# Kernel tuning notes

Measured on AMD Instinct MI355X. Metric: run time of the kernel, lower is better.

## Reference

```python
import jax, jax.numpy as jnp
import numpy as np
import math

# dims matching init_kwargs
B, N, CS, CZ = 1, 512, 384, 128
H, C, PQ, PV = 8, 128, 8, 8
INF, EPS = 1e5, 1e-8

# ---- quaternion / motor helpers (PGA motor encoded as [qw,qx,qy,qz,tx,ty,tz,0]) ----

def quat_conj(q):
    return q * jnp.array([1.0, -1.0, -1.0, -1.0], q.dtype)

def quat_mul(a, b):
    aw, ax, ay, az = jnp.split(a, 4, -1)
    bw, bx, by, bz = jnp.split(b, 4, -1)
    return jnp.concatenate([
        aw*bw - ax*bx - ay*by - az*bz,
        aw*bx + ax*bw + ay*bz - az*by,
        aw*by - ax*bz + ay*bw + az*bx,
        aw*bz + ax*by - ay*bx + az*bw], -1)

def quat_rotate(q, v):
    qv = q[..., 1:]
    uv = jnp.cross(qv, v)
    uuv = jnp.cross(qv, uv)
    return v + 2.0 * (q[..., :1] * uv + uuv)

def point_trafo(p, q, t):
    # p [...,K,3]; rigid transform by frame motor, homogeneous 4-vector out
    pp = quat_rotate(q, p) + t
    return jnp.concatenate([pp, jnp.ones_like(pp[..., :1])], -1)

def mv_transform(mv, q, t):
    # versor sandwich on a 16-dim multivector: three rotatable 3-vector blocks,
    # the point block (7:10, weight at 10) also translates; slots 0 and 10:16 invariant
    s0 = mv[..., 0:1]
    v1 = quat_rotate(q, mv[..., 1:4])
    v2 = quat_rotate(q, mv[..., 4:7])
    w = mv[..., 10:11]
    p = quat_rotate(q, mv[..., 7:10]) + w * t
    return jnp.concatenate([s0, v1, v2, p, mv[..., 10:16]], -1)

def mv_transform_inv(mv, q, t):
    qc = quat_conj(q)
    s0 = mv[..., 0:1]
    v1 = quat_rotate(qc, mv[..., 1:4])
    v2 = quat_rotate(qc, mv[..., 4:7])
    w = mv[..., 10:11]
    p = quat_rotate(qc, mv[..., 7:10] - w * t)
    return jnp.concatenate([s0, v1, v2, p, mv[..., 10:16]], -1)


def _forward(s, g, z, T, mask, W_q, b_q, W_kv, b_kv, W_qp, b_qp, W_kp, b_kp,
             W_vg, b_vg, W_mg, W_b, b_b, W_dz, b_dz, head_weights,
             softmax_weights, W_out, b_out, W_geo):
    T8 = T[..., :8]                                      # extract_motor
    qn = T8[..., :4]
    qn = qn / jnp.sqrt(jnp.sum(qn**2, -1, keepdims=True) + EPS)
    tr = T8[..., 4:7]

    q = (s @ W_q + b_q).reshape(B, N, H, C)
    kv = (s @ W_kv + b_kv).reshape(B, N, H, 2 * C)
    k, v = kv[..., :C], kv[..., C:]

    def make_pts(W, bb):
        # split into 3 chunks + stack(dim=-1) == reshape(...,3,HP).swapaxes
        p = (s @ W + bb).reshape(B, N, 3, H * PQ).swapaxes(-1, -2)  # [B,N,HP,3]
        p4 = point_trafo(p, qn[:, :, None, :], tr[:, :, None, :])
        return p4.reshape(B, N, H, PQ, 4)

    q_pts = make_pts(W_qp, b_qp)
    k_pts = make_pts(W_kp, b_kp)

    v_g = (s @ W_vg + b_vg).reshape(B, N, PV, 16)
    v_g = jnp.einsum('oi,bnic->bnoc', W_mg,
                     jnp.concatenate([v_g, g], -2)).reshape(B, N, H, PV, 16)

    bias = jnp.einsum('bijz,zh->bhij', z, W_b) + b_b[None, :, None, None]
    a = jnp.einsum('bihc,bjhc->bhij', q, k) * math.sqrt(1.0 / (3 * C))
    a = a + math.sqrt(1.0 / 3.0) * bias

    disp = q_pts[:, :, None, :, :, :3] - k_pts[:, None, :, :, :, :3]  # [B,N,N,H,P,3]
    pt = jnp.sum(disp**2, -1)                                         # [B,N,N,H,P]
    hw = jax.nn.softplus(head_weights) * math.sqrt(1.0 / (3 * (PQ * 9.0 / 2)))
    pt = -0.5 * jnp.sum(pt * hw[None, None, None, :, None], -1)       # [B,N,N,H]

    sq_mask = INF * (mask[:, :, None] * mask[:, None, :] - 1.0)
    a = a + pt.transpose(0, 3, 1, 2) + sq_mask[:, None]
    a = jax.nn.softmax(softmax_weights[None, :, None, None] * a, axis=-1)

    o = jnp.einsum('bhij,bjhc->bihc', a, v)                           # [B,N,H,C]

    qb, tb = qn[:, :, None, None, :], tr[:, :, None, None, :]
    vg_glob = mv_transform(v_g, qb, tb)
    o_g = jnp.einsum('bhij,bjhpc->bihpc', a, vg_glob)
    o_g = mv_transform_inv(o_g, qb, tb)                               # [B,N,H,PV,16]
    n1 = jnp.sqrt(jnp.sum(o_g[..., :10]**2, -1) + EPS)
    n2 = jnp.sqrt(jnp.sum(o_g[..., 10:]**2, -1) + EPS)
    o_g_norm = jnp.stack([n1, n2], -1)                                # [B,N,H,PV,2]

    # local relative frame features (8 per head)
    q_rel = quat_mul(quat_conj(qn)[:, :, None, :], qn[:, None, :, :])
    t_rel = quat_rotate(quat_conj(qn)[:, :, None, :], tr[:, None, :, :] - tr[:, :, None, :])
    rel = jnp.concatenate([q_rel, t_rel, jnp.zeros_like(t_rel[..., :1])], -1)  # [B,N,N,8]
    o_rel = jnp.einsum('bhij,bijc->bihc', a, rel)

    o_pair = jnp.einsum('bhij,bijc->bihc', a, z @ W_dz + b_dz)        # [B,N,H,CZ//4]

    feats = jnp.concatenate([o_pair, o, o_rel,
                             o_g.reshape(B, N, H, PV * 16),
                             o_g_norm.reshape(B, N, H, PV * 2)], -1).reshape(B, N, -1)
    s_out = feats @ W_out + b_out                                     # [B,N,CS]
    g_out = jnp.einsum('oi,bnic->bnoc', W_geo, o_g.reshape(B, N, H * PV, 16))
    return s_out, g_out


def setup_inputs() -> dict:
    key = jax.random.key(0)
    ks = jax.random.split(key, 32)
    def rn(i, shape, sc=1.0):
        return sc * jax.random.normal(ks[i], shape, jnp.float32)
    s = rn(0, (B, N, CS))
    g = rn(1, (B, N, PV, 16))
    z = rn(2, (B, N, N, CZ))
    Traw = rn(3, (B, N, 16))
    qn = Traw[..., :4]
    qn = qn / jnp.sqrt(jnp.sum(qn**2, -1, keepdims=True) + 1e-8)
    T = Traw.at[..., :4].set(qn).at[..., 4:7].multiply(3.0).at[..., 7:].set(0.0)
    mask = jnp.ones((B, N), jnp.float32)
    w = 0.02
    CAT = H * (CZ // 4 + C + 8 + PV * 18)   # 2496
    return dict(
        s=s, g=g, z=z, T=T, mask=mask,
        W_q=rn(4, (CS, H * C), w), b_q=jnp.zeros((H * C,), jnp.float32),
        W_kv=rn(5, (CS, 2 * H * C), w), b_kv=jnp.zeros((2 * H * C,), jnp.float32),
        W_qp=rn(6, (CS, H * PQ * 3), w), b_qp=jnp.zeros((H * PQ * 3,), jnp.float32),
        W_kp=rn(7, (CS, H * PQ * 3), w), b_kp=jnp.zeros((H * PQ * 3,), jnp.float32),
        W_vg=rn(8, (CS, PV * 16), w), b_vg=jnp.zeros((PV * 16,), jnp.float32),
        W_mg=rn(9, (H * PV, 2 * PV), 0.1),
        W_b=rn(10, (CZ, H), w), b_b=jnp.zeros((H,), jnp.float32),
        W_dz=rn(11, (CZ, CZ // 4), w), b_dz=jnp.zeros((CZ // 4,), jnp.float32),
        head_weights=-2.0 + 0.3 * rn(12, (H,)),
        softmax_weights=jnp.ones((H,), jnp.float32) + 0.1 * rn(13, (H,)),
        W_out=rn(14, (CAT, CS), w), b_out=jnp.zeros((CS,), jnp.float32),
        W_geo=rn(15, (PV, H * PV), 0.1))


def reference(s, g, z, T, mask, W_q, b_q, W_kv, b_kv, W_qp, b_qp, W_kp, b_kp,
              W_vg, b_vg, W_mg, W_b, b_b, W_dz, b_dz, head_weights,
              softmax_weights, W_out, b_out, W_geo):
    return _forward(s, g, z, T, mask, W_q, b_q, W_kv, b_kv, W_qp, b_qp, W_kp,
                    b_kp, W_vg, b_vg, W_mg, W_b, b_b, W_dz, b_dz, head_weights,
                    softmax_weights, W_out, b_out, W_geo)
```

## Files before the change

### kernel.cpp

```cpp
#include <hip/hip_runtime.h>
#include <math.h>

#define NN 512
#define CSD 384
#define CZD 128
#define HD 8
#define CD 128
#define EPSV 1e-8f
#define INFV 100000.0f

#define OFF_QN    ((size_t)0)
#define OFF_TR    ((size_t)2048)
#define OFF_ROWT  ((size_t)4096)
#define OFF_COLT  ((size_t)8192)
#define OFF_SB    ((size_t)12288)
#define OFF_QBUF  ((size_t)45056)
#define OFF_KV    ((size_t)569344)
#define OFF_QPR   ((size_t)1617920)
#define OFF_KPR   ((size_t)1716224)
#define OFF_VGR   ((size_t)1814528)
#define OFF_ZB    ((size_t)1880064)
#define OFF_A     ((size_t)3977216)
#define OFF_AMH   ((size_t)6074368)
#define OFF_AML   ((size_t)7122944)
#define OFF_UH    ((size_t)8171520)
#define OFF_UL    ((size_t)8499200)
#define OFF_VH    ((size_t)8826880)
#define OFF_VL    ((size_t)9154560)
#define OFF_VPH   ((size_t)9482240)
#define OFF_VPL   ((size_t)10006528)
#define OFF_OB0   ((size_t)10530816)
#define OFF_OB1   ((size_t)11055104)
#define OFF_OG0   ((size_t)11579392)
#define OFF_OG1   ((size_t)12103680)
#define OFF_FH    ((size_t)12627968)
#define OFF_FL    ((size_t)13266944)
#define OFF_PS    ((size_t)13905920)
#define OFF_SH    ((size_t)15085568)
#define OFF_SL    ((size_t)15183872)
#define OFF_WTH   ((size_t)15282176)
#define OFF_WTL   ((size_t)15970304)
#define OFF_WOH   ((size_t)16658432)
#define OFF_WOL   ((size_t)17137664)

typedef __attribute__((ext_vector_type(4))) float f32x4;
typedef __attribute__((ext_vector_type(8))) short bf16x8;
typedef __attribute__((ext_vector_type(4))) short s16x4;
typedef unsigned short u16;

__device__ __forceinline__ void qrot(const float q[4], const float* v, float* out) {
    float qw = q[0], qx = q[1], qy = q[2], qz = q[3];
    float ux = qy*v[2] - qz*v[1];
    float uy = qz*v[0] - qx*v[2];
    float uz = qx*v[1] - qy*v[0];
    float uux = qy*uz - qz*uy;
    float uuy = qz*ux - qx*uz;
    float uuz = qx*uy - qy*ux;
    out[0] = v[0] + 2.0f*(qw*ux + uux);
    out[1] = v[1] + 2.0f*(qw*uy + uuy);
    out[2] = v[2] + 2.0f*(qw*uz + uuz);
}

__device__ __forceinline__ void cvt2(float x, u16& h, u16& lo) {
    unsigned u = __float_as_uint(x);
    unsigned r = (u + 0x7FFFu + ((u >> 16) & 1u)) >> 16;
    h = (u16)r;
    float hf = __uint_as_float(r << 16);
    float lf = x - hf;
    unsigned u2 = __float_as_uint(lf);
    unsigned r2 = (u2 + 0x7FFFu + ((u2 >> 16) & 1u)) >> 16;
    lo = (u16)r2;
}
__device__ __forceinline__ float bf2f(u16 h) { return __uint_as_float((unsigned)h << 16); }

#define MFMA3(acc, avh, avl, bvh, bvl) \
    acc = __builtin_amdgcn_mfma_f32_16x16x32_bf16(avh, bvh, acc, 0, 0, 0); \
    acc = __builtin_amdgcn_mfma_f32_16x16x32_bf16(avh, bvl, acc, 0, 0, 0); \
    acc = __builtin_amdgcn_mfma_f32_16x16x32_bf16(avl, bvh, acc, 0, 0, 0);


__global__ __launch_bounds__(256) void k_split(
    const float* __restrict__ s, const float* __restrict__ W_q, const float* __restrict__ W_kv,
    const float* __restrict__ W_qp, const float* __restrict__ W_kp, const float* __restrict__ W_vg,
    const float* __restrict__ W_out,
    u16* __restrict__ sh_, u16* __restrict__ sl_,
    u16* __restrict__ WTh, u16* __restrict__ WTl,
    u16* __restrict__ WOh, u16* __restrict__ WOl)
{
    __shared__ float tile[64*68];
    int task = blockIdx.z, bx = blockIdx.x, by = blockIdx.y, t = threadIdx.x;
    if (task == 0) {
        if (by >= 6) return;
        const float* W; int ldn, sn0;
        if (bx < 16)      { W = W_q;  ldn = 1024; sn0 = bx*64; }
        else if (bx < 48) { W = W_kv; ldn = 2048; sn0 = (bx-16)*64; }
        else if (bx < 51) { W = W_qp; ldn = 192;  sn0 = (bx-48)*64; }
        else if (bx < 54) { W = W_kp; ldn = 192;  sn0 = (bx-51)*64; }
        else              { W = W_vg; ldn = 128;  sn0 = (bx-54)*64; }
        int k0 = by*64;
        #pragma unroll
        for (int lp = 0; lp < 4; lp++) {
            int kk = (t>>4) + lp*16, nn = (t&15)*4;
            float4 v = *(const float4*)(W + (size_t)(k0+kk)*ldn + sn0 + nn);
            tile[kk*68+nn]=v.x; tile[kk*68+nn+1]=v.y; tile[kk*68+nn+2]=v.z; tile[kk*68+nn+3]=v.w;
        }
        __syncthreads();
        #pragma unroll
        for (int lp = 0; lp < 4; lp++) {
            int nn = (t>>4) + lp*16, kk4 = (t&15)*4;
            s16x4 vh, vl;
            #pragma unroll
            for (int e = 0; e < 4; e++) {
                u16 h, lo; cvt2(tile[(kk4+e)*68 + nn], h, lo);
                vh[e] = (short)h; vl[e] = (short)lo;
            }
            size_t o = (size_t)(bx*64 + nn)*384 + k0 + kk4;
            *(s16x4*)(WTh + o) = vh;
            *(s16x4*)(WTl + o) = vl;
        }
    } else if (task == 1) {
        if (bx >= 6 || by >= 39) return;
        int n0 = bx*64, k0 = by*64;
        #pragma unroll
        for (int lp = 0; lp < 4; lp++) {
            int kk = (t>>4) + lp*16, nn = (t&15)*4;
            float4 v = *(const float4*)(W_out + (size_t)(k0+kk)*384 + n0 + nn);
            tile[kk*68+nn]=v.x; tile[kk*68+nn+1]=v.y; tile[kk*68+nn+2]=v.z; tile[kk*68+nn+3]=v.w;
        }
        __syncthreads();
        #pragma unroll
        for (int lp = 0; lp < 4; lp++) {
            int nn = (t>>4) + lp*16, kk4 = (t&15)*4;
            s16x4 vh, vl;
            #pragma unroll
            for (int e = 0; e < 4; e++) {
                u16 h, lo; cvt2(tile[(kk4+e)*68 + nn], h, lo);
                vh[e] = (short)h; vl[e] = (short)lo;
            }
            size_t o = (size_t)(n0 + nn)*2496 + k0 + kk4;
            *(s16x4*)(WOh + o) = vh;
            *(s16x4*)(WOl + o) = vl;
        }
    } else {
        if (bx >= 8 || by >= 6) return;
        int m0 = bx*64, k0 = by*64;
        #pragma unroll
        for (int lp = 0; lp < 4; lp++) {
            int row = (t>>4) + lp*16, c4 = (t&15)*4;
            float4 v = *(const float4*)(s + (size_t)(m0+row)*384 + k0 + c4);
            s16x4 vh, vl;
            u16 h, lo;
            cvt2(v.x,h,lo); vh[0]=(short)h; vl[0]=(short)lo;
            cvt2(v.y,h,lo); vh[1]=(short)h; vl[1]=(short)lo;
            cvt2(v.z,h,lo); vh[2]=(short)h; vl[2]=(short)lo;
            cvt2(v.w,h,lo); vh[3]=(short)h; vl[3]=(short)lo;
            size_t o = (size_t)(m0+row)*384 + k0 + c4;
            *(s16x4*)(sh_ + o) = vh;
            *(s16x4*)(sl_ + o) = vl;
        }
    }
}

__global__ __launch_bounds__(256) void k_proj_all(
    const u16* __restrict__ sh_, const u16* __restrict__ sl_,
    const u16* __restrict__ WTh, const u16* __restrict__ WTl,
    const float* __restrict__ b_q,  float* __restrict__ qbuf,
    const float* __restrict__ b_kv, float* __restrict__ kvb,
    const float* __restrict__ b_qp, float* __restrict__ qpr,
    const float* __restrict__ b_kp, float* __restrict__ kpr,
    const float* __restrict__ b_vg, float* __restrict__ vgr)
{
    int ny = blockIdx.y;
    const float* bias; float* C; int N, n0, base;
    if (ny < 16)      { bias=b_q;  C=qbuf; N=1024; n0=ny*64;      base=0; }
    else if (ny < 48) { bias=b_kv; C=kvb;  N=2048; n0=(ny-16)*64; base=1024; }
    else if (ny < 51) { bias=b_qp; C=qpr;  N=192;  n0=(ny-48)*64; base=3072; }
    else if (ny < 54) { bias=b_kp; C=kpr;  N=192;  n0=(ny-51)*64; base=3264; }
    else              { bias=b_vg; C=vgr;  N=128;  n0=(ny-54)*64; base=3456; }
    int m0 = blockIdx.x*64;
    int t = threadIdx.x, w = t>>6, l = t&63, g = l>>4, li = l&15;
    const u16* Ah = sh_ + (size_t)(m0 + w*16 + li)*384 + g*8;
    const u16* Al = sl_ + (size_t)(m0 + w*16 + li)*384 + g*8;
    const u16* Bh0 = WTh + (size_t)(base + n0 + li)*384 + g*8;
    const u16* Bl0 = WTl + (size_t)(base + n0 + li)*384 + g*8;
    f32x4 acc[4] = {};
    for (int ks = 0; ks < 12; ks++) {
        bf16x8 avh = *(const bf16x8*)(Ah + ks*32);
        bf16x8 avl = *(const bf16x8*)(Al + ks*32);
        #pragma unroll
        for (int c = 0; c < 4; c++) {
            bf16x8 bvh = *(const bf16x8*)(Bh0 + (size_t)c*16*384 + ks*32);
            bf16x8 bvl = *(const bf16x8*)(Bl0 + (size_t)c*16*384 + ks*32);
            MFMA3(acc[c], avh, avl, bvh, bvl);
        }
    }
    #pragma unroll
    for (int c = 0; c < 4; c++) {
        int col = n0 + c*16 + li;
        float bb = bias[col];
        #pragma unroll
        for (int r = 0; r < 4; r++) {
            int row = m0 + w*16 + g*4 + r;
            C[(size_t)row*N + col] = acc[c][r] + bb;
        }
    }
}

__global__ __launch_bounds__(256) void k_geo(
    const float* __restrict__ T,
    const float* __restrict__ qpr, const float* __restrict__ kpr,
    const float* __restrict__ vgr, const float* __restrict__ g,
    const float* __restrict__ W_mg,
    const float* __restrict__ qbuf, const float* __restrict__ kvb,
    const float* __restrict__ hwraw, const float* __restrict__ b_b,
    float* __restrict__ qn, float* __restrict__ tr,
    u16* __restrict__ Uh, u16* __restrict__ Ul,
    u16* __restrict__ Vh, u16* __restrict__ Vl,
    float* __restrict__ rowt, float* __restrict__ colt,
    u16* __restrict__ Vph, u16* __restrict__ Vpl)
{
    __shared__ float s_q[4];
    __shared__ float s_t[3];
    __shared__ float s_qpts[192], s_kpts[192];
    __shared__ float s_Qsq[8], s_Ksq[8];
    int n = blockIdx.x, t = threadIdx.x;
    if (t == 0) {
        float q0=T[n*16+0], q1=T[n*16+1], q2=T[n*16+2], q3=T[n*16+3];
        float inv = 1.0f/sqrtf(q0*q0+q1*q1+q2*q2+q3*q3 + EPSV);
        float a0=q0*inv, a1=q1*inv, a2=q2*inv, a3=q3*inv;
        s_q[0]=a0; s_q[1]=a1; s_q[2]=a2; s_q[3]=a3;
        float u0=T[n*16+4], u1=T[n*16+5], u2=T[n*16+6];
        s_t[0]=u0; s_t[1]=u1; s_t[2]=u2;
        qn[n*4+0]=a0; qn[n*4+1]=a1; qn[n*4+2]=a2; qn[n*4+3]=a3;
        tr[n*3+0]=u0; tr[n*3+1]=u1; tr[n*3+2]=u2;
    }
    __syncthreads();
    float q[4]={s_q[0],s_q[1],s_q[2],s_q[3]};
    float t0=s_t[0], t1=s_t[1], t2=s_t[2];
    if (t < 128) {
        int m = t & 63;
        const float* raw = (t < 64) ? qpr : kpr;
        float p[3] = {raw[n*192 + m], raw[n*192 + 64 + m], raw[n*192 + 128 + m]};
        float r[3]; qrot(q,p,r);
        r[0]+=t0; r[1]+=t1; r[2]+=t2;
        float* dp = (t<64) ? s_qpts : s_kpts;
        dp[m*3+0]=r[0]; dp[m*3+1]=r[1]; dp[m*3+2]=r[2];
        float ss = r[0]*r[0]+r[1]*r[1]+r[2]*r[2];
        ss += __shfl_down(ss,4,8);
        ss += __shfl_down(ss,2,8);
        ss += __shfl_down(ss,1,8);
        if ((m&7)==0) ((t<64)?s_Qsq:s_Ksq)[m>>3] = ss;
    } else if (t < 192) {
        int o = t - 128;
        float in[16];
        #pragma unroll
        for (int c=0;c<16;c++){
            float acc=0.0f;
            #pragma unroll
            for (int i=0;i<8;i++)  acc += W_mg[o*16+i]*vgr[n*128+i*16+c];
            #pragma unroll
            for (int i=8;i<16;i++) acc += W_mg[o*16+i]*g[n*128+(i-8)*16+c];
            in[c]=acc;
        }
        float out[16];
        out[0]=in[0];
        qrot(q,in+1,out+1);
        qrot(q,in+4,out+4);
        float w=in[10];
        qrot(q,in+7,out+7);
        out[7]+=w*t0; out[8]+=w*t1; out[9]+=w*t2;
        #pragma unroll
        for (int c=10;c<16;c++) out[c]=in[c];
        int h=o>>3, pp=o&7;
        size_t vb = ((size_t)(h*512+n))*256 + 128 + pp*16;
        #pragma unroll
        for (int c=0;c<16;c++) {
            u16 hh, ll; cvt2(out[c], hh, ll);
            Vph[vb+c]=hh; Vpl[vb+c]=ll;
        }
    }
    #pragma unroll
    for (int l=0;l<4;l++){
        int f = t + l*256; int h = f>>7, c = f&127;
        u16 hh, ll; cvt2(kvb[(size_t)n*2048 + h*256 + 128 + c], hh, ll);
        Vph[((size_t)(h*512+n))*256 + c] = hh;
        Vpl[((size_t)(h*512+n))*256 + c] = ll;
    }
    __syncthreads();
    #pragma unroll
    for (int h = 0; h < 8; h++) {
        float hwv = log1pf(expf(hwraw[h])) * 0.09622504486493763f;
        if (t < 160) {
            float u, v;
            if (t < 128) {
                u = 0.05103103630798287f * qbuf[(size_t)n*1024 + h*128 + t];
                v = kvb[(size_t)n*2048 + h*256 + t];
            } else if (t < 152) {
                int d = t - 128;
                u = hwv * s_qpts[h*24 + d];
                v = s_kpts[h*24 + d];
            } else { u = 0.0f; v = 0.0f; }
            size_t o = ((size_t)h*512 + n)*160 + t;
            u16 hh, ll;
            cvt2(u, hh, ll); Uh[o]=hh; Ul[o]=ll;
            cvt2(v, hh, ll); Vh[o]=hh; Vl[o]=ll;
        }
        if (t == 160) rowt[h*512+n] = -0.5f*hwv*s_Qsq[h] + 0.5773502691896258f*b_b[h] - INFV;
        if (t == 161) colt[h*512+n] = -0.5f*hwv*s_Ksq[h];
    }
}

__global__ __launch_bounds__(128) void k_zb(const float* __restrict__ z,
        const float* __restrict__ W_b, float* __restrict__ zb) {
    __shared__ float zt[64*132];
    __shared__ float part[8*64];
    int i = blockIdx.x, j0 = blockIdx.y*64;
    int t = threadIdx.x;
    #pragma unroll
    for (int l = 0; l < 16; l++) {
        int f = t + l*128;
        int row = f >> 5, c4 = (f & 31) << 2;
        float4 v = *(const float4*)(z + ((size_t)(i*NN) + j0 + row)*CZD + c4);
        *(float4*)(zt + row*132 + c4) = v;
    }
    __syncthreads();
    int w = t >> 6, j = t & 63;
    int cbase = w*64;
    float acc[8] = {};
    #pragma unroll
    for (int c16 = 0; c16 < 16; c16++) {
        float4 v = *(const float4*)(zt + j*132 + cbase + c16*4);
        int c = cbase + c16*4;
        #pragma unroll
        for (int h = 0; h < 8; h++)
            acc[h] += v.x*W_b[(c+0)*8+h] + v.y*W_b[(c+1)*8+h]
                    + v.z*W_b[(c+2)*8+h] + v.w*W_b[(c+3)*8+h];
    }
    if (w == 1) {
        #pragma unroll
        for (int h = 0; h < 8; h++) part[h*64 + j] = acc[h];
    }
    __syncthreads();
    if (w == 0) {
        #pragma unroll
        for (int h = 0; h < 8; h++)
            zb[((size_t)h*512 + i)*512 + j0 + j] = acc[h] + part[h*64 + j];
    }
}

__global__ __launch_bounds__(256) void k_scorefill(
        const u16* __restrict__ Uh, const u16* __restrict__ Ul,
        const u16* __restrict__ Vh, const u16* __restrict__ Vl,
        const float* __restrict__ rowt, const float* __restrict__ colt,
        const float* __restrict__ zb, const float* __restrict__ mask,
        const float* __restrict__ sw, float* __restrict__ Am) {
    int h = blockIdx.z;
    int m0 = blockIdx.x*64, n0 = blockIdx.y*64;
    int t = threadIdx.x, w = t>>6, l = t&63, g = l>>4, li = l&15;
    const u16* Ah = Uh + ((size_t)h*512 + m0 + w*16 + li)*160 + g*8;
    const u16* Al = Ul + ((size_t)h*512 + m0 + w*16 + li)*160 + g*8;
    const u16* Bh0 = Vh + ((size_t)h*512 + n0 + li)*160 + g*8;
    const u16* Bl0 = Vl + ((size_t)h*512 + n0 + li)*160 + g*8;
    f32x4 acc[4] = {};
    #pragma unroll
    for (int ks = 0; ks < 5; ks++) {
        bf16x8 avh = *(const bf16x8*)(Ah + ks*32);
        bf16x8 avl = *(const bf16x8*)(Al + ks*32);
        #pragma unroll
        for (int c = 0; c < 4; c++) {
            bf16x8 bvh = *(const bf16x8*)(Bh0 + (size_t)c*16*160 + ks*32);
            bf16x8 bvl = *(const bf16x8*)(Bl0 + (size_t)c*16*160 + ks*32);
            MFMA3(acc[c], avh, avl, bvh, bvl);
        }
    }
    float swh = sw[h];
    #pragma unroll
    for (int c = 0; c < 4; c++) {
        int j = n0 + c*16 + li;
        float ct = colt[h*512 + j];
        float mj = mask[j];
        #pragma unroll
        for (int r = 0; r < 4; r++) {
            int i = m0 + w*16 + g*4 + r;
            float rt = rowt[h*512 + i];
            float mi = mask[i]*INFV;
            float zv = zb[((size_t)h*512 + i)*512 + j];
            Am[((size_t)h*512 + i)*512 + j] =
                (acc[c][r] + rt + ct + 0.5773502691896258f*zv + mi*mj)*swh;
        }
    }
}

__global__ __launch_bounds__(256) void k_softmax(const float* __restrict__ Am,
        u16* __restrict__ Amh, u16* __restrict__ Aml,
        const float* __restrict__ qn, const float* __restrict__ tr, float* __restrict__ S) {
    __shared__ float red[8];
    __shared__ float sred[4][8];
    int row = blockIdx.x;
    const float* p = Am + (size_t)row*512;
    int t = threadIdx.x;
    float x0 = p[t], x1 = p[t+256];
    float m = fmaxf(x0, x1);
    #pragma unroll
    for (int o = 32; o > 0; o >>= 1) m = fmaxf(m, __shfl_xor(m, o));
    int wv = t >> 6, ln = t & 63;
    if (ln == 0) red[wv] = m;
    __syncthreads();
    m = fmaxf(fmaxf(red[0], red[1]), fmaxf(red[2], red[3]));
    float e0 = expf(x0 - m), e1 = expf(x1 - m);
    float sm = e0 + e1;
    #pragma unroll
    for (int o = 32; o > 0; o >>= 1) sm += __shfl_xor(sm, o);
    __syncthreads();
    if (ln == 0) red[4 + wv] = sm;
    __syncthreads();
    float inv = 1.0f / (red[4]+red[5]+red[6]+red[7]);
    float a0 = e0*inv, a1 = e1*inv;
    u16 hh, ll;
    cvt2(a0, hh, ll); Amh[(size_t)row*512 + t] = hh;     Aml[(size_t)row*512 + t] = ll;
    cvt2(a1, hh, ll); Amh[(size_t)row*512 + t+256] = hh; Aml[(size_t)row*512 + t+256] = ll;
    float4 q0 = *(const float4*)(qn + t*4);
    float4 q1 = *(const float4*)(qn + (t+256)*4);
    float acc[8];
    acc[0] = a0*q0.x + a1*q1.x;
    acc[1] = a0*q0.y + a1*q1.y;
    acc[2] = a0*q0.z + a1*q1.z;
    acc[3] = a0*q0.w + a1*q1.w;
    acc[4] = a0*tr[t*3+0] + a1*tr[(t+256)*3+0];
    acc[5] = a0*tr[t*3+1] + a1*tr[(t+256)*3+1];
    acc[6] = a0*tr[t*3+2] + a1*tr[(t+256)*3+2];
    acc[7] = a0 + a1;
    #pragma unroll
    for (int c = 0; c < 8; c++) {
        #pragma unroll
        for (int o = 32; o > 0; o >>= 1) acc[c] += __shfl_xor(acc[c], o);
    }
    if (ln == 0) {
        #pragma unroll
        for (int c = 0; c < 8; c++) sred[wv][c] = acc[c];
    }
    __syncthreads();
    if (t < 8) {
        int h = row >> 9, i = row & 511;
        S[i*64 + h*8 + t] = sred[0][t]+sred[1][t]+sred[2][t]+sred[3][t];
    }
}

__global__ __launch_bounds__(256) void k_apply(
        const u16* __restrict__ Amh, const u16* __restrict__ Aml,
        const u16* __restrict__ Vph, const u16* __restrict__ Vpl,
        float* __restrict__ ob0, float* __restrict__ ob1,
        float* __restrict__ og0, float* __restrict__ og1) {
    __shared__ u16 sBh[2][64*48];
    __shared__ u16 sBl[2][64*48];
    int m0 = blockIdx.x*64;
    int n0 = blockIdx.y*64;
    int h = blockIdx.z & 7, js = blockIdx.z >> 3;
    int t = threadIdx.x, w = t>>6, l = t&63, g = l>>4, li = l&15;
    int jl = t>>3, c8 = (t&7)*8;
    int jsw = jl ^ (((c8>>3)&3)<<3);
    const u16* Ah = Amh + ((size_t)h*512 + m0 + w*16 + li)*512 + js*256 + g*8;
    const u16* Al = Aml + ((size_t)h*512 + m0 + w*16 + li)*512 + js*256 + g*8;
    f32x4 acc[4] = {};
    {
        const u16* srcH = Vph + ((size_t)h*512 + js*256 + jl)*256 + n0 + c8;
        const u16* srcL = Vpl + ((size_t)h*512 + js*256 + jl)*256 + n0 + c8;
        bf16x8 vh = *(const bf16x8*)srcH;
        bf16x8 vl = *(const bf16x8*)srcL;
        #pragma unroll
        for (int e = 0; e < 8; e++) {
            sBh[0][(c8+e)*48 + jsw] = (u16)vh[e];
            sBl[0][(c8+e)*48 + jsw] = (u16)vl[e];
        }
    }
    __syncthreads();
    for (int kc = 0; kc < 8; kc++) {
        int cur = kc & 1;
        if (kc + 1 < 8) {
            int koff = js*256 + (kc+1)*32;
            const u16* srcH = Vph + ((size_t)h*512 + koff + jl)*256 + n0 + c8;
            const u16* srcL = Vpl + ((size_t)h*512 + koff + jl)*256 + n0 + c8;
            bf16x8 vh = *(const bf16x8*)srcH;
            bf16x8 vl = *(const bf16x8*)srcL;
            #pragma unroll
            for (int e = 0; e < 8; e++) {
                sBh[cur^1][(c8+e)*48 + jsw] = (u16)vh[e];
                sBl[cur^1][(c8+e)*48 + jsw] = (u16)vl[e];
            }
        }
        bf16x8 avh = *(const bf16x8*)(Ah + kc*32);
        bf16x8 avl = *(const bf16x8*)(Al + kc*32);
        #pragma unroll
        for (int c = 0; c < 4; c++) {
            int col = c*16 + li;
            int gp = g ^ ((col>>3)&3);
            bf16x8 bvh = *(const bf16x8*)(&sBh[cur][col*48 + gp*8]);
            bf16x8 bvl = *(const bf16x8*)(&sBl[cur][col*48 + gp*8]);
            MFMA3(acc[c], avh, avl, bvh, bvl);
        }
        __syncthreads();
    }
    float* obuf = js ? ob1 : ob0;
    float* og   = js ? og1 : og0;
    #pragma unroll
    for (int c = 0; c < 4; c++) {
        int col = n0 + c*16 + li;
        float* base = (col < 128) ? (obuf + h*128 + col) : (og + h*128 + col - 128);
        #pragma unroll
        for (int r = 0; r < 4; r++) {
            int i = m0 + w*16 + g*4 + r;
            base[(size_t)i*1024] = acc[c][r];
        }
    }
}

__global__ __launch_bounds__(256) void k_azfin(
    const u16* __restrict__ Amh, const u16* __restrict__ Aml, const float* __restrict__ z,
    const float* __restrict__ ob0, const float* __restrict__ ob1,
    const float* __restrict__ og0, const float* __restrict__ og1,
    const float* __restrict__ W_dz, const float* __restrict__ b_dz,
    const float* __restrict__ S, const float* __restrict__ qn, const float* __restrict__ tr,
    const float* __restrict__ W_geo,
    u16* __restrict__ fh, u16* __restrict__ fl, float* __restrict__ outg)
{
    __shared__ float aT[512*8];
    __shared__ float part[3*1024];
    __shared__ float s_az[1024];
    __shared__ float s_og[1024];
    int i = blockIdx.x, t = threadIdx.x;
    #pragma unroll
    for (int l = 0; l < 16; l++) {
        int f = t + l*256;
        int h = f >> 9, j = f & 511;
        size_t idx = ((size_t)h*512 + i)*512 + j;
        aT[j*8 + h] = bf2f(Amh[idx]) + bf2f(Aml[idx]);
    }
    __syncthreads();
    int c2 = t & 63, quarter = t >> 6;
    int jb = quarter*128;
    float acc[8][2] = {};
    for (int j = jb; j < jb+128; j++) {
        float2 zv = *(const float2*)(z + ((size_t)(i*NN) + j)*CZD + c2*2);
        float4 a0 = *(const float4*)(aT + j*8);
        float4 a1 = *(const float4*)(aT + j*8 + 4);
        acc[0][0] += a0.x*zv.x; acc[0][1] += a0.x*zv.y;
        acc[1][0] += a0.y*zv.x; acc[1][1] += a0.y*zv.y;
        acc[2][0] += a0.z*zv.x; acc[2][1] += a0.z*zv.y;
        acc[3][0] += a0.w*zv.x; acc[3][1] += a0.w*zv.y;
        acc[4][0] += a1.x*zv.x; acc[4][1] += a1.x*zv.y;
        acc[5][0] += a1.y*zv.x; acc[5][1] += a1.y*zv.y;
        acc[6][0] += a1.z*zv.x; acc[6][1] += a1.z*zv.y;
        acc[7][0] += a1.w*zv.x; acc[7][1] += a1.w*zv.y;
    }
    if (quarter > 0) {
        #pragma unroll
        for (int h = 0; h < 8; h++) {
            part[(quarter-1)*1024 + h*128 + c2*2 + 0] = acc[h][0];
            part[(quarter-1)*1024 + h*128 + c2*2 + 1] = acc[h][1];
        }
    }
    __syncthreads();
    if (quarter == 0) {
        #pragma unroll
        for (int h = 0; h < 8; h++) {
            #pragma unroll
            for (int d = 0; d < 2; d++) {
                s_az[h*128 + c2*2 + d] = acc[h][d] + part[h*128 + c2*2 + d]
                          + part[1024 + h*128 + c2*2 + d] + part[2048 + h*128 + c2*2 + d];
            }
        }
    }
    __syncthreads();
    size_t fb = (size_t)i*2496;
    u16 hh, ll;
    #pragma unroll
    for (int l = 0; l < 4; l++) {
        int ff = t + l*256; int h = ff>>7, c = ff&127;
        float v = ob0[(size_t)i*1024 + h*128 + c] + ob1[(size_t)i*1024 + h*128 + c];
        cvt2(v, hh, ll); fh[fb + h*312 + 32 + c] = hh; fl[fb + h*312 + 32 + c] = ll;
    }
    {
        int h = t >> 5, cdz = t & 31;
        float a2 = b_dz[cdz];
        #pragma unroll 4
        for (int zc = 0; zc < 128; zc++) a2 += s_az[h*128 + zc]*W_dz[zc*32 + cdz];
        cvt2(a2, hh, ll); fh[fb + h*312 + cdz] = hh; fl[fb + h*312 + cdz] = ll;
    }
    float qc0=qn[i*4], qc1=-qn[i*4+1], qc2=-qn[i*4+2], qc3=-qn[i*4+3];
    float t0=tr[i*3], t1=tr[i*3+1], t2=tr[i*3+2];
    if (t < 64) {
        int h = t >> 3, p = t & 7;
        const float* a0 = og0 + (size_t)i*1024 + h*128 + p*16;
        const float* a1 = og1 + (size_t)i*1024 + h*128 + p*16;
        float in[16];
        #pragma unroll
        for (int c=0;c<16;c++) in[c]=a0[c]+a1[c];
        float qc[4]={qc0,qc1,qc2,qc3};
        float out[16];
        out[0]=in[0];
        qrot(qc,in+1,out+1);
        qrot(qc,in+4,out+4);
        float w=in[10];
        float tmp[3]={in[7]-w*t0, in[8]-w*t1, in[9]-w*t2};
        qrot(qc,tmp,out+7);
        #pragma unroll
        for (int c2x=10;c2x<16;c2x++) out[c2x]=in[c2x];
        float n1=EPSV, n2=EPSV;
        #pragma unroll
        for (int c2x=0;c2x<10;c2x++) n1 += out[c2x]*out[c2x];
        #pragma unroll
        for (int c2x=10;c2x<16;c2x++) n2 += out[c2x]*out[c2x];
        n1=sqrtf(n1); n2=sqrtf(n2);
        #pragma unroll
        for (int c2x=0;c2x<16;c2x++){
            cvt2(out[c2x], hh, ll);
            fh[fb + h*312+168+p*16+c2x] = hh; fl[fb + h*312+168+p*16+c2x] = ll;
            s_og[t*16+c2x]=out[c2x];
        }
// ... 40 lines not shown
    const u16* Al = fl + (size_t)(m0 + w*16 + li)*2496 + kz*416 + g*8;
    const u16* Bh0 = WOh + (size_t)(n0 + li)*2496 + kz*416 + g*8;
    const u16* Bl0 = WOl + (size_t)(n0 + li)*2496 + kz*416 + g*8;
    f32x4 acc[4] = {};
    for (int ks = 0; ks < 13; ks++) {
        bf16x8 avh = *(const bf16x8*)(Ah + ks*32);
        bf16x8 avl = *(const bf16x8*)(Al + ks*32);
        #pragma unroll
        for (int c = 0; c < 4; c++) {
            bf16x8 bvh = *(const bf16x8*)(Bh0 + (size_t)c*16*2496 + ks*32);
            bf16x8 bvl = *(const bf16x8*)(Bl0 + (size_t)c*16*2496 + ks*32);
            MFMA3(acc[c], avh, avl, bvh, bvl);
        }
    }
    float* slab = Ps + (size_t)kz*512*384;
    #pragma unroll
    for (int c = 0; c < 4; c++) {
        int col = n0 + c*16 + li;
        #pragma unroll
        for (int r = 0; r < 4; r++) {
            int row = m0 + w*16 + g*4 + r;
            slab[(size_t)row*CSD + col] = acc[c][r];
        }
    }
}

__global__ __launch_bounds__(256) void k_sout_red(const float* __restrict__ Ps,
        const float* __restrict__ b_out, float* __restrict__ out) {
    int idx = (blockIdx.x*256 + threadIdx.x)*4;
    float4 s = *(const float4*)(b_out + (idx % 384));
    #pragma unroll
    for (int kz = 0; kz < 6; kz++) {
        float4 p = *(const float4*)(Ps + (size_t)kz*196608 + idx);
        s.x += p.x; s.y += p.y; s.z += p.z; s.w += p.w;
    }
    *(float4*)(out + idx) = s;
}


extern "C" void kernel_launch(void* const* d_in, const int* in_sizes, int n_in,
                              void* d_out, int out_size, void* d_ws, size_t ws_size,
                              hipStream_t stream) {
    const float* s     = (const float*)d_in[0];
    const float* g     = (const float*)d_in[1];
    const float* z     = (const float*)d_in[2];
    const float* T     = (const float*)d_in[3];
    const float* mask  = (const float*)d_in[4];
    const float* W_q   = (const float*)d_in[5];
    const float* b_q   = (const float*)d_in[6];
    const float* W_kv  = (const float*)d_in[7];
    const float* b_kv  = (const float*)d_in[8];
    const float* W_qp  = (const float*)d_in[9];
    const float* b_qp  = (const float*)d_in[10];
    const float* W_kp  = (const float*)d_in[11];
    const float* b_kp  = (const float*)d_in[12];
    const float* W_vg  = (const float*)d_in[13];
    const float* b_vg  = (const float*)d_in[14];
    const float* W_mg  = (const float*)d_in[15];
    const float* W_b   = (const float*)d_in[16];
    const float* b_b   = (const float*)d_in[17];
    const float* W_dz  = (const float*)d_in[18];
    const float* b_dz  = (const float*)d_in[19];
    const float* hw    = (const float*)d_in[20];
    const float* sw    = (const float*)d_in[21];
    const float* W_out = (const float*)d_in[22];
    const float* b_out = (const float*)d_in[23];
    const float* W_geo = (const float*)d_in[24];

    float* ws   = (float*)d_ws;
    float* out  = (float*)d_out;

    float* qn   = ws + OFF_QN;
    float* tr   = ws + OFF_TR;
    float* rowt = ws + OFF_ROWT;
    float* colt = ws + OFF_COLT;
    float* Sbuf = ws + OFF_SB;
    float* qbuf = ws + OFF_QBUF;
    float* kvb  = ws + OFF_KV;
    float* qpr  = ws + OFF_QPR;
    float* kpr  = ws + OFF_KPR;
    float* vgr  = ws + OFF_VGR;
    float* zb   = ws + OFF_ZB;
    float* Am   = ws + OFF_A;
    u16* Amh    = (u16*)(ws + OFF_AMH);
    u16* Aml    = (u16*)(ws + OFF_AML);
    u16* Uh     = (u16*)(ws + OFF_UH);
    u16* Ul     = (u16*)(ws + OFF_UL);
    u16* Vh     = (u16*)(ws + OFF_VH);
    u16* Vl     = (u16*)(ws + OFF_VL);
    u16* Vph    = (u16*)(ws + OFF_VPH);
    u16* Vpl    = (u16*)(ws + OFF_VPL);
    float* ob0  = ws + OFF_OB0;
    float* ob1  = ws + OFF_OB1;
    float* og0  = ws + OFF_OG0;
    float* og1  = ws + OFF_OG1;
    u16* fh     = (u16*)(ws + OFF_FH);
    u16* fl     = (u16*)(ws + OFF_FL);
    float* Ps   = ws + OFF_PS;
    u16* sh_    = (u16*)(ws + OFF_SH);
    u16* sl_    = (u16*)(ws + OFF_SL);
    u16* WTh    = (u16*)(ws + OFF_WTH);
    u16* WTl    = (u16*)(ws + OFF_WTL);
    u16* WOh    = (u16*)(ws + OFF_WOH);
    u16* WOl    = (u16*)(ws + OFF_WOL);

    k_split<<<dim3(56,39,3),256,0,stream>>>(s,W_q,W_kv,W_qp,W_kp,W_vg,W_out,
                                            sh_,sl_,WTh,WTl,WOh,WOl);
    k_proj_all<<<dim3(8,56),256,0,stream>>>(sh_,sl_,WTh,WTl,
                                            b_q,qbuf, b_kv,kvb, b_qp,qpr, b_kp,kpr, b_vg,vgr);
    k_geo<<<NN,256,0,stream>>>(T,qpr,kpr,vgr,g,W_mg,qbuf,kvb,hw,b_b,
                               qn,tr,Uh,Ul,Vh,Vl,rowt,colt,Vph,Vpl);
    k_zb<<<dim3(NN,8),128,0,stream>>>(z,W_b,zb);
    k_scorefill<<<dim3(8,8,8),256,0,stream>>>(Uh,Ul,Vh,Vl,rowt,colt,zb,mask,sw,Am);
    k_softmax<<<4096,256,0,stream>>>(Am,Amh,Aml,qn,tr,Sbuf);
    k_apply<<<dim3(8,4,16),256,0,stream>>>(Amh,Aml,Vph,Vpl,ob0,ob1,og0,og1);
    k_azfin<<<NN,256,0,stream>>>(Amh,Aml,z,ob0,ob1,og0,og1,W_dz,b_dz,Sbuf,qn,tr,W_geo,
                                 fh,fl, out + (size_t)NN*CSD);
    k_sout<<<dim3(8,6,6),256,0,stream>>>(fh,fl,WOh,WOl,Ps);
    k_sout_red<<<192,256,0,stream>>>(Ps,b_out,out);
}
```

Measured before the change: 409.6 us.

## Keep attention intermediates in fp32 and split to bf16 hi/lo inside MFMA tiles

Stops writing pre-split bf16 hi/lo copies of U, V, Vp and the attention matrix to global memory. The score and apply kernels now share a templated tile routine that loads fp32 tiles, splits them into hi/lo in LDS and runs three-pass bf16 MFMA with register prefetch. Softmax writes probabilities back in place, which removes the separate hi/lo arrays. k_zb is rewritten to hold W_b in registers and reduce with shuffles. The change trades global traffic for extra conversion work and LDS staging in the GEMM kernels, with the conversion now repeated for every tile that reads the same data.

```diff
diff --git a/kernel.cpp b/kernel.cpp
--- a/kernel.cpp
+++ b/kernel.cpp
@@ -21,27 +21,22 @@
 #define OFF_VGR   ((size_t)1814528)
 #define OFF_ZB    ((size_t)1880064)
 #define OFF_A     ((size_t)3977216)
-#define OFF_AMH   ((size_t)6074368)
-#define OFF_AML   ((size_t)7122944)
-#define OFF_UH    ((size_t)8171520)
-#define OFF_UL    ((size_t)8499200)
-#define OFF_VH    ((size_t)8826880)
-#define OFF_VL    ((size_t)9154560)
-#define OFF_VPH   ((size_t)9482240)
-#define OFF_VPL   ((size_t)10006528)
-#define OFF_OB0   ((size_t)10530816)
-#define OFF_OB1   ((size_t)11055104)
-#define OFF_OG0   ((size_t)11579392)
-#define OFF_OG1   ((size_t)12103680)
-#define OFF_FH    ((size_t)12627968)
-#define OFF_FL    ((size_t)13266944)
-#define OFF_PS    ((size_t)13905920)
-#define OFF_SH    ((size_t)15085568)
-#define OFF_SL    ((size_t)15183872)
-#define OFF_WTH   ((size_t)15282176)
-#define OFF_WTL   ((size_t)15970304)
-#define OFF_WOH   ((size_t)16658432)
-#define OFF_WOL   ((size_t)17137664)
+#define OFF_U     ((size_t)6074368)
+#define OFF_V     ((size_t)6729728)
+#define OFF_VP    ((size_t)7385088)
+#define OFF_OB0   ((size_t)8433664)
+#define OFF_OB1   ((size_t)8957952)
+#define OFF_OG0   ((size_t)9482240)
+#define OFF_OG1   ((size_t)10006528)
+#define OFF_PS    ((size_t)10530816)
+#define OFF_SH    ((size_t)11710464)
+#define OFF_SL    ((size_t)11808768)
+#define OFF_WTH   ((size_t)11907072)
+#define OFF_WTL   ((size_t)12595200)
+#define OFF_WOH   ((size_t)13283328)
+#define OFF_WOL   ((size_t)13762560)
+#define OFF_FH    ((size_t)14241792)
+#define OFF_FL    ((size_t)14880768)
 
 typedef __attribute__((ext_vector_type(4))) float f32x4;
 typedef __attribute__((ext_vector_type(8))) short bf16x8;
@@ -71,12 +66,79 @@
     unsigned r2 = (u2 + 0x7FFFu + ((u2 >> 16) & 1u)) >> 16;
     lo = (u16)r2;
 }
-__device__ __forceinline__ float bf2f(u16 h) { return __uint_as_float((unsigned)h << 16); }
 
 #define MFMA3(acc, avh, avl, bvh, bvl) \
     acc = __builtin_amdgcn_mfma_f32_16x16x32_bf16(avh, bvh, acc, 0, 0, 0); \
     acc = __builtin_amdgcn_mfma_f32_16x16x32_bf16(avh, bvl, acc, 0, 0, 0); \
     acc = __builtin_amdgcn_mfma_f32_16x16x32_bf16(avl, bvh, acc, 0, 0, 0);
+
+__device__ __forceinline__ void stA(short* H, short* L, int row, int k4, float4 v) {
+    u16 h0,l0,h1,l1,h2,l2,h3,l3;
+    cvt2(v.x,h0,l0); cvt2(v.y,h1,l1); cvt2(v.z,h2,l2); cvt2(v.w,h3,l3);
+    s16x4 vh = {(short)h0,(short)h1,(short)h2,(short)h3};
+    s16x4 vl = {(short)l0,(short)l1,(short)l2,(short)l3};
+    *(s16x4*)(H + row*40 + k4) = vh;
+    *(s16x4*)(L + row*40 + k4) = vl;
+}
+__device__ __forceinline__ void stBT(short* H, short* L, int k, int n4, float4 v) {
+    u16 h, lo;
+    cvt2(v.x,h,lo); H[(n4+0)*40+k]=(short)h; L[(n4+0)*40+k]=(short)lo;
+    cvt2(v.y,h,lo); H[(n4+1)*40+k]=(short)h; L[(n4+1)*40+k]=(short)lo;
+    cvt2(v.z,h,lo); H[(n4+2)*40+k]=(short)h; L[(n4+2)*40+k]=(short)lo;
+    cvt2(v.w,h,lo); H[(n4+3)*40+k]=(short)h; L[(n4+3)*40+k]=(short)lo;
+}
+
+template<int BT>
+__device__ __forceinline__ void mfma_tiles(const float* __restrict__ A, int lda,
+                                           const float* __restrict__ B, int ldb,
+                                           int m0, int n0, int k0, int nk,
+                                           f32x4* acc,
+                                           short* Ah, short* Al, short* Bh, short* Bl) {
+    int t = threadIdx.x;
+    int w = t >> 6, l = t & 63, g = l >> 4, li = l & 15;
+    int ar = t >> 3, ak = (t & 7) << 2;
+    const float* Ap0 = A + (size_t)(m0 + ar)*lda + ak;
+    const float* Ap1 = A + (size_t)(m0 + ar + 32)*lda + ak;
+    const float* Bp0; const float* Bp1;
+    int bk = t >> 4, bn = (t & 15) << 2;
+    if (BT) {
+        Bp0 = B + (size_t)(n0 + ar)*ldb + ak;
+        Bp1 = B + (size_t)(n0 + ar + 32)*ldb + ak;
+    } else {
+        Bp0 = B + (size_t)bk*ldb + n0 + bn;
+        Bp1 = B + (size_t)(bk + 16)*ldb + n0 + bn;
+    }
+    float4 a0 = *(const float4*)(Ap0 + k0);
+    float4 a1 = *(const float4*)(Ap1 + k0);
+    float4 b0, b1;
+    if (BT) { b0 = *(const float4*)(Bp0 + k0); b1 = *(const float4*)(Bp1 + k0); }
+    else    { b0 = *(const float4*)(Bp0 + (size_t)k0*ldb); b1 = *(const float4*)(Bp1 + (size_t)k0*ldb); }
+    for (int kc = 0; kc < nk; kc++) {
+        stA(Ah, Al, ar, ak, a0);
+        stA(Ah, Al, ar+32, ak, a1);
+        if (BT) { stA(Bh, Bl, ar, ak, b0); stA(Bh, Bl, ar+32, ak, b1); }
+        else    { stBT(Bh, Bl, bk, bn, b0); stBT(Bh, Bl, bk+16, bn, b1); }
+        __syncthreads();
+        if (kc + 1 < nk) {
+            int kb = k0 + (kc+1)*32;
+            a0 = *(const float4*)(Ap0 + kb);
+            a1 = *(const float4*)(Ap1 + kb);
+            if (BT) { b0 = *(const float4*)(Bp0 + kb); b1 = *(const float4*)(Bp1 + kb); }
+            else { b0 = *(const float4*)(Bp0 + (size_t)kb*ldb); b1 = *(const float4*)(Bp1 + (size_t)kb*ldb); }
+        }
+        int arow = (w*16 + li)*40 + g*8;
+        bf16x8 avh = *(bf16x8*)(Ah + arow);
+        bf16x8 avl = *(bf16x8*)(Al + arow);
+        #pragma unroll
+        for (int c = 0; c < 4; c++) {
+            int brow = (c*16 + li)*40 + g*8;
+            bf16x8 bvh = *(bf16x8*)(Bh + brow);
+            bf16x8 bvl = *(bf16x8*)(Bl + brow);
+            MFMA3(acc[c], avh, avl, bvh, bvl);
+        }
+        __syncthreads();
+    }
+}
 
 
 __global__ __launch_bounds__(256) void k_split(
@@ -214,10 +276,9 @@
     const float* __restrict__ qbuf, const float* __restrict__ kvb,
     const float* __restrict__ hwraw, const float* __restrict__ b_b,
     float* __restrict__ qn, float* __restrict__ tr,
-    u16* __restrict__ Uh, u16* __restrict__ Ul,
-    u16* __restrict__ Vh, u16* __restrict__ Vl,
+    float* __restrict__ U, float* __restrict__ V,
     float* __restrict__ rowt, float* __restrict__ colt,
-    u16* __restrict__ Vph, u16* __restrict__ Vpl)
+    float* __restrict__ Vp)
 {
     __shared__ float s_q[4];
     __shared__ float s_t[3];
@@ -272,19 +333,14 @@
         #pragma unroll
         for (int c=10;c<16;c++) out[c]=in[c];
         int h=o>>3, pp=o&7;
-        size_t vb = ((size_t)(h*512+n))*256 + 128 + pp*16;
-        #pragma unroll
-        for (int c=0;c<16;c++) {
-            u16 hh, ll; cvt2(out[c], hh, ll);
-            Vph[vb+c]=hh; Vpl[vb+c]=ll;
-        }
+        float* vp = Vp + ((size_t)(h*512+n))*256 + 128 + pp*16;
+        #pragma unroll
+        for (int c=0;c<16;c++) vp[c]=out[c];
     }
     #pragma unroll
     for (int l=0;l<4;l++){
         int f = t + l*256; int h = f>>7, c = f&127;
-        u16 hh, ll; cvt2(kvb[(size_t)n*2048 + h*256 + 128 + c], hh, ll);
-        Vph[((size_t)(h*512+n))*256 + c] = hh;
-        Vpl[((size_t)(h*512+n))*256 + c] = ll;
+        Vp[((size_t)(h*512+n))*256 + c] = kvb[(size_t)n*2048 + h*256 + 128 + c];
     }
     __syncthreads();
     #pragma unroll
@@ -300,79 +356,65 @@
                 u = hwv * s_qpts[h*24 + d];
                 v = s_kpts[h*24 + d];
             } else { u = 0.0f; v = 0.0f; }
-            size_t o = ((size_t)h*512 + n)*160 + t;
-            u16 hh, ll;
-            cvt2(u, hh, ll); Uh[o]=hh; Ul[o]=ll;
-            cvt2(v, hh, ll); Vh[o]=hh; Vl[o]=ll;
+            U[((size_t)h*512 + n)*160 + t] = u;
+            V[((size_t)h*512 + n)*160 + t] = v;
         }
         if (t == 160) rowt[h*512+n] = -0.5f*hwv*s_Qsq[h] + 0.5773502691896258f*b_b[h] - INFV;
         if (t == 161) colt[h*512+n] = -0.5f*hwv*s_Ksq[h];
     }
 }
 
-__global__ __launch_bounds__(128) void k_zb(const float* __restrict__ z,
+__global__ __launch_bounds__(256) void k_zb(const float* __restrict__ z,
         const float* __restrict__ W_b, float* __restrict__ zb) {
-    __shared__ float zt[64*132];
-    __shared__ float part[8*64];
-    int i = blockIdx.x, j0 = blockIdx.y*64;
-    int t = threadIdx.x;
-    #pragma unroll
-    for (int l = 0; l < 16; l++) {
-        int f = t + l*128;
-        int row = f >> 5, c4 = (f & 31) << 2;
-        float4 v = *(const float4*)(z + ((size_t)(i*NN) + j0 + row)*CZD + c4);
-        *(float4*)(zt + row*132 + c4) = v;
-    }
-    __syncthreads();
-    int w = t >> 6, j = t & 63;
-    int cbase = w*64;
-    float acc[8] = {};
-    #pragma unroll
-    for (int c16 = 0; c16 < 16; c16++) {
-        float4 v = *(const float4*)(zt + j*132 + cbase + c16*4);
-        int c = cbase + c16*4;
-        #pragma unroll
-        for (int h = 0; h < 8; h++)
-            acc[h] += v.x*W_b[(c+0)*8+h] + v.y*W_b[(c+1)*8+h]
-                    + v.z*W_b[(c+2)*8+h] + v.w*W_b[(c+3)*8+h];
-    }
-    if (w == 1) {
-        #pragma unroll
-        for (int h = 0; h < 8; h++) part[h*64 + j] = acc[h];
-    }
-    __syncthreads();
-    if (w == 0) {
-        #pragma unroll
-        for (int h = 0; h < 8; h++)
-            zb[((size_t)h*512 + i)*512 + j0 + j] = acc[h] + part[h*64 + j];
-    }
-}
-
-__global__ __launch_bounds__(256) void k_scorefill(
-        const u16* __restrict__ Uh, const u16* __restrict__ Ul,
-        const u16* __restrict__ Vh, const u16* __restrict__ Vl,
+    int i = blockIdx.x, j0 = blockIdx.y*128;
+    int t = threadIdx.x, w = t>>6, l = t&63;
+    int gp = l>>4, k = l&15;
+    float wb[8][8];
+    #pragma unroll
+    for (int cc=0;cc<8;cc++){
+        float4 w0 = *(const float4*)(W_b + (k*8+cc)*8);
+        float4 w1 = *(const float4*)(W_b + (k*8+cc)*8 + 4);
+        wb[cc][0]=w0.x; wb[cc][1]=w0.y; wb[cc][2]=w0.z; wb[cc][3]=w0.w;
+        wb[cc][4]=w1.x; wb[cc][5]=w1.y; wb[cc][6]=w1.z; wb[cc][7]=w1.w;
+    }
+    for (int it = 0; it < 8; it++) {
+        int j = j0 + it*16 + w*4 + gp;
+        const float* zp = z + ((size_t)i*512 + j)*128 + k*8;
+        float4 za = *(const float4*)(zp);
+        float4 zb4 = *(const float4*)(zp + 4);
+        float zz[8] = {za.x,za.y,za.z,za.w,zb4.x,zb4.y,zb4.z,zb4.w};
+        float acc[8];
+        #pragma unroll
+        for (int h=0;h<8;h++) acc[h] = zz[0]*wb[0][h];
+        #pragma unroll
+        for (int cc=1;cc<8;cc++)
+            #pragma unroll
+            for (int h=0;h<8;h++) acc[h] += zz[cc]*wb[cc][h];
+        #pragma unroll
+        for (int h=0;h<8;h++) {
+            acc[h] += __shfl_xor(acc[h], 1);
+            acc[h] += __shfl_xor(acc[h], 2);
+            acc[h] += __shfl_xor(acc[h], 4);
+            acc[h] += __shfl_xor(acc[h], 8);
+        }
+        float outv = acc[0];
+        #pragma unroll
+        for (int h=1;h<8;h++) if (k == h) outv = acc[h];
+        if (k < 8) zb[((size_t)k*512 + i)*512 + j] = outv;
+    }
+}
+
+__global__ __launch_bounds__(256) void k_scorefill(const float* __restrict__ U, const float* __restrict__ V,
         const float* __restrict__ rowt, const float* __restrict__ colt,
         const float* __restrict__ zb, const float* __restrict__ mask,
         const float* __restrict__ sw, float* __restrict__ Am) {
+    __shared__ short Ah[64*40], Al[64*40], Bh[64*40], Bl[64*40];
     int h = blockIdx.z;
     int m0 = blockIdx.x*64, n0 = blockIdx.y*64;
-    int t = threadIdx.x, w = t>>6, l = t&63, g = l>>4, li = l&15;
-    const u16* Ah = Uh + ((size_t)h*512 + m0 + w*16 + li)*160 + g*8;
-    const u16* Al = Ul + ((size_t)h*512 + m0 + w*16 + li)*160 + g*8;
-    const u16* Bh0 = Vh + ((size_t)h*512 + n0 + li)*160 + g*8;
-    const u16* Bl0 = Vl + ((size_t)h*512 + n0 + li)*160 + g*8;
     f32x4 acc[4] = {};
-    #pragma unroll
-    for (int ks = 0; ks < 5; ks++) {
-        bf16x8 avh = *(const bf16x8*)(Ah + ks*32);
-        bf16x8 avl = *(const bf16x8*)(Al + ks*32);
-        #pragma unroll
-        for (int c = 0; c < 4; c++) {
-            bf16x8 bvh = *(const bf16x8*)(Bh0 + (size_t)c*16*160 + ks*32);
-            bf16x8 bvl = *(const bf16x8*)(Bl0 + (size_t)c*16*160 + ks*32);
-            MFMA3(acc[c], avh, avl, bvh, bvl);
-        }
-    }
+    mfma_tiles<1>(U + (size_t)h*512*160, 160, V + (size_t)h*512*160, 160,
+                  m0, n0, 0, 5, acc, Ah, Al, Bh, Bl);
+    int t = threadIdx.x, w = t >> 6, l = t & 63, g = l >> 4, li = l & 15;
     float swh = sw[h];
     #pragma unroll
     for (int c = 0; c < 4; c++) {
@@ -391,13 +433,12 @@
     }
 }
 
-__global__ __launch_bounds__(256) void k_softmax(const float* __restrict__ Am,
-        u16* __restrict__ Amh, u16* __restrict__ Aml,
+__global__ __launch_bounds__(256) void k_softmax(float* __restrict__ Am,
         const float* __restrict__ qn, const float* __restrict__ tr, float* __restrict__ S) {
     __shared__ float red[8];
     __shared__ float sred[4][8];
     int row = blockIdx.x;
-    const float* p = Am + (size_t)row*512;
+    float* p = Am + (size_t)row*512;
     int t = threadIdx.x;
     float x0 = p[t], x1 = p[t+256];
     float m = fmaxf(x0, x1);
@@ -416,9 +457,8 @@
     __syncthreads();
     float inv = 1.0f / (red[4]+red[5]+red[6]+red[7]);
     float a0 = e0*inv, a1 = e1*inv;
-    u16 hh, ll;
-    cvt2(a0, hh, ll); Amh[(size_t)row*512 + t] = hh;     Aml[(size_t)row*512 + t] = ll;
-    cvt2(a1, hh, ll); Amh[(size_t)row*512 + t+256] = hh; Aml[(size_t)row*512 + t+256] = ll;
+    p[t] = a0;
+    p[t+256] = a1;
     float4 q0 = *(const float4*)(qn + t*4);
     float4 q1 = *(const float4*)(qn + (t+256)*4);
     float acc[8];
@@ -446,60 +486,17 @@
     }
 }
 
-__global__ __launch_bounds__(256) void k_apply(
-        const u16* __restrict__ Amh, const u16* __restrict__ Aml,
-        const u16* __restrict__ Vph, const u16* __restrict__ Vpl,
-        float* __restrict__ ob0, float* __restrict__ ob1,
+__global__ __launch_bounds__(256) void k_apply(const float* __restrict__ Am,
+        const float* __restrict__ Vp, float* __restrict__ ob0, float* __restrict__ ob1,
         float* __restrict__ og0, float* __restrict__ og1) {
-    __shared__ u16 sBh[2][64*48];
-    __shared__ u16 sBl[2][64*48];
+    __shared__ short Ah[64*40], Al[64*40], Bh[64*40], Bl[64*40];
     int m0 = blockIdx.x*64;
     int n0 = blockIdx.y*64;
     int h = blockIdx.z & 7, js = blockIdx.z >> 3;
-    int t = threadIdx.x, w = t>>6, l = t&63, g = l>>4, li = l&15;
-    int jl = t>>3, c8 = (t&7)*8;
-    int jsw = jl ^ (((c8>>3)&3)<<3);
-    const u16* Ah = Amh + ((size_t)h*512 + m0 + w*16 + li)*512 + js*256 + g*8;
-    const u16* Al = Aml + ((size_t)h*512 + m0 + w*16 + li)*512 + js*256 + g*8;
     f32x4 acc[4] = {};
-    {
-        const u16* srcH = Vph + ((size_t)h*512 + js*256 + jl)*256 + n0 + c8;
-        const u16* srcL = Vpl + ((size_t)h*512 + js*256 + jl)*256 + n0 + c8;
-        bf16x8 vh = *(const bf16x8*)srcH;
-        bf16x8 vl = *(const bf16x8*)srcL;
-        #pragma unroll
-        for (int e = 0; e < 8; e++) {
-            sBh[0][(c8+e)*48 + jsw] = (u16)vh[e];
-            sBl[0][(c8+e)*48 + jsw] = (u16)vl[e];
-        }
-    }
-    __syncthreads();
-    for (int kc = 0; kc < 8; kc++) {
-        int cur = kc & 1;
-        if (kc + 1 < 8) {
-            int koff = js*256 + (kc+1)*32;
-            const u16* srcH = Vph + ((size_t)h*512 + koff + jl)*256 + n0 + c8;
-            const u16* srcL = Vpl + ((size_t)h*512 + koff + jl)*256 + n0 + c8;
-            bf16x8 vh = *(const bf16x8*)srcH;
-            bf16x8 vl = *(const bf16x8*)srcL;
-            #pragma unroll
-            for (int e = 0; e < 8; e++) {
-                sBh[cur^1][(c8+e)*48 + jsw] = (u16)vh[e];
-                sBl[cur^1][(c8+e)*48 + jsw] = (u16)vl[e];
-            }
-        }
-        bf16x8 avh = *(const bf16x8*)(Ah + kc*32);
-        bf16x8 avl = *(const bf16x8*)(Al + kc*32);
-        #pragma unroll
-        for (int c = 0; c < 4; c++) {
-            int col = c*16 + li;
-            int gp = g ^ ((col>>3)&3);
-            bf16x8 bvh = *(const bf16x8*)(&sBh[cur][col*48 + gp*8]);
-            bf16x8 bvl = *(const bf16x8*)(&sBl[cur][col*48 + gp*8]);
-            MFMA3(acc[c], avh, avl, bvh, bvl);
-        }
-        __syncthreads();
-    }
+    mfma_tiles<0>(Am + (size_t)h*512*512, 512, Vp + (size_t)h*512*256, 256,
+                  m0, n0, js*256, 8, acc, Ah, Al, Bh, Bl);
+    int t = threadIdx.x, w = t >> 6, l = t & 63, g = l >> 4, li = l & 15;
     float* obuf = js ? ob1 : ob0;
     float* og   = js ? og1 : og0;
     #pragma unroll
@@ -515,7 +512,7 @@
 }
 
 __global__ __launch_bounds__(256) void k_azfin(
-    const u16* __restrict__ Amh, const u16* __restrict__ Aml, const float* __restrict__ z,
+    const float* __restrict__ Am, const float* __restrict__ z,
     const float* __restrict__ ob0, const float* __restrict__ ob1,
     const float* __restrict__ og0, const float* __restrict__ og1,
     const float* __restrict__ W_dz, const float* __restrict__ b_dz,
@@ -532,8 +529,7 @@
     for (int l = 0; l < 16; l++) {
         int f = t + l*256;
         int h = f >> 9, j = f & 511;
-        size_t idx = ((size_t)h*512 + i)*512 + j;
-        aT[j*8 + h] = bf2f(Amh[idx]) + bf2f(Aml[idx]);
+        aT[j*8 + h] = Am[((size_t)h*512 + i)*512 + j];
     }
     __syncthreads();
     int c2 = t & 63, quarter = t >> 6;
@@ -740,20 +736,13 @@
     float* vgr  = ws + OFF_VGR;
     float* zb   = ws + OFF_ZB;
     float* Am   = ws + OFF_A;
-    u16* Amh    = (u16*)(ws + OFF_AMH);
-    u16* Aml    = (u16*)(ws + OFF_AML);
-    u16* Uh     = (u16*)(ws + OFF_UH);
-    u16* Ul     = (u16*)(ws + OFF_UL);
-    u16* Vh     = (u16*)(ws + OFF_VH);
-    u16* Vl     = (u16*)(ws + OFF_VL);
-    u16* Vph    = (u16*)(ws + OFF_VPH);
-    u16* Vpl    = (u16*)(ws + OFF_VPL);
+    float* U    = ws + OFF_U;
+    float* V    = ws + OFF_V;
+    float* Vp   = ws + OFF_VP;
     float* ob0  = ws + OFF_OB0;
     float* ob1  = ws + OFF_OB1;
     float* og0  = ws + OFF_OG0;
     float* og1  = ws + OFF_OG1;
-    u16* fh     = (u16*)(ws + OFF_FH);
-    u16* fl     = (u16*)(ws + OFF_FL);
     float* Ps   = ws + OFF_PS;
     u16* sh_    = (u16*)(ws + OFF_SH);
     u16* sl_    = (u16*)(ws + OFF_SL);
@@ -761,18 +750,20 @@
     u16* WTl    = (u16*)(ws + OFF_WTL);
     u16* WOh    = (u16*)(ws + OFF_WOH);
     u16* WOl    = (u16*)(ws + OFF_WOL);
+    u16* fh     = (u16*)(ws + OFF_FH);
+    u16* fl     = (u16*)(ws + OFF_FL);
 
     k_split<<<dim3(56,39,3),256,0,stream>>>(s,W_q,W_kv,W_qp,W_kp,W_vg,W_out,
                                             sh_,sl_,WTh,WTl,WOh,WOl);
     k_proj_all<<<dim3(8,56),256,0,stream>>>(sh_,sl_,WTh,WTl,
                                             b_q,qbuf, b_kv,kvb, b_qp,qpr, b_kp,kpr, b_vg,vgr);
     k_geo<<<NN,256,0,stream>>>(T,qpr,kpr,vgr,g,W_mg,qbuf,kvb,hw,b_b,
-                               qn,tr,Uh,Ul,Vh,Vl,rowt,colt,Vph,Vpl);
-    k_zb<<<dim3(NN,8),128,0,stream>>>(z,W_b,zb);
-    k_scorefill<<<dim3(8,8,8),256,0,stream>>>(Uh,Ul,Vh,Vl,rowt,colt,zb,mask,sw,Am);
-    k_softmax<<<4096,256,0,stream>>>(Am,Amh,Aml,qn,tr,Sbuf);
-    k_apply<<<dim3(8,4,16),256,0,stream>>>(Amh,Aml,Vph,Vpl,ob0,ob1,og0,og1);
-    k_azfin<<<NN,256,0,stream>>>(Amh,Aml,z,ob0,ob1,og0,og1,W_dz,b_dz,Sbuf,qn,tr,W_geo,
+                               qn,tr,U,V,rowt,colt,Vp);
+    k_zb<<<dim3(512,4),256,0,stream>>>(z,W_b,zb);
+    k_scorefill<<<dim3(8,8,8),256,0,stream>>>(U,V,rowt,colt,zb,mask,sw,Am);
+    k_softmax<<<4096,256,0,stream>>>(Am,qn,tr,Sbuf);
+    k_apply<<<dim3(8,4,16),256,0,stream>>>(Am,Vp,ob0,ob1,og0,og1);
+    k_azfin<<<NN,256,0,stream>>>(Am,z,ob0,ob1,og0,og1,W_dz,b_dz,Sbuf,qn,tr,W_geo,
                                  fh,fl, out + (size_t)NN*CSD);
     k_sout<<<dim3(8,6,6),256,0,stream>>>(fh,fl,WOh,WOl,Ps);
     k_sout_red<<<192,256,0,stream>>>(Ps,b_out,out);
```

Measured after the change: 404.2 us. No clear change (-1.3%).
